# Kernel optimization log

Hardware: AMD Instinct MI355X
Metric: run time of the kernel (lower is better)

## Reference

```python
import jax, jax.numpy as jnp
import numpy as np

RES_W, RES_H = 256, 256
MAX_SAMPLES = 384
TF_RES = 128
FOV_DEG = 30.0
NEAR, FAR = 0.1, 100.0
BG = 0.0
HIT_EPS = 1e-3


def _normalize(v, axis=-1):
    return v / jnp.linalg.norm(v, axis=axis, keepdims=True)


def trilinear_sample(vol, tex):
    # vol: [X,Y,Z], tex: [...,3] in voxel coordinates
    res = np.array(vol.shape, dtype=np.float32)
    p = jnp.clip(tex, 0.0, jnp.asarray(res - 1.0 - 1e-6, jnp.float32))
    lo = jnp.floor(p).astype(jnp.int32)
    f = p - lo.astype(p.dtype)
    hi = jnp.minimum(lo + 1, jnp.asarray(res.astype(np.int32) - 1))
    x0, y0, z0 = lo[..., 0], lo[..., 1], lo[..., 2]
    x1, y1, z1 = hi[..., 0], hi[..., 1], hi[..., 2]
    fx, fy, fz = f[..., 0], f[..., 1], f[..., 2]
    c000 = vol[x0, y0, z0]; c100 = vol[x1, y0, z0]
    c010 = vol[x0, y1, z0]; c110 = vol[x1, y1, z0]
    c001 = vol[x0, y0, z1]; c101 = vol[x1, y0, z1]
    c011 = vol[x0, y1, z1]; c111 = vol[x1, y1, z1]
    c00 = c000 * (1 - fx) + c100 * fx
    c10 = c010 * (1 - fx) + c110 * fx
    c01 = c001 * (1 - fx) + c101 * fx
    c11 = c011 * (1 - fx) + c111 * fx
    c0 = c00 * (1 - fy) + c10 * fy
    c1 = c01 * (1 - fy) + c11 * fy
    return c0 * (1 - fz) + c1 * fz


def tf_lookup(tf, x):
    # tf: [T,4], x: [...] intensity in [0,1]
    T = tf.shape[0]
    xi = jnp.clip(x, 0.0, 1.0) * (T - 1)
    lo = jnp.floor(xi).astype(jnp.int32)
    hi = jnp.minimum(lo + 1, T - 1)
    f = (xi - lo.astype(xi.dtype))[..., None]
    return tf[lo] * (1 - f) + tf[hi] * f


def render_one(vol, tf, cam, sr):
    # vol [X,Y,Z], tf [T,4], cam [3] -> [W,H,5] (rgba + depth)
    W, H = RES_W, RES_H
    fwd = _normalize(-cam)
    world_up = jnp.array([0.0, 1.0, 0.0], jnp.float32)
    right = _normalize(jnp.cross(fwd, world_up))
    up = jnp.cross(right, fwd)
    tanf = jnp.tan(jnp.float32(np.radians(FOV_DEG) / 2))
    aspect = W / H
    u = ((jnp.arange(W) + 0.5) / W * 2 - 1) * tanf * aspect  # [W]
    v = ((jnp.arange(H) + 0.5) / H * 2 - 1) * tanf           # [H]
    dirs = fwd + u[:, None, None] * right + v[None, :, None] * up  # [W,H,3]
    dirs = _normalize(dirs)
    # ray-box intersection against [-1,1]^3
    inv = 1.0 / dirs
    t_lo = (-1.0 - cam) * inv
    t_hi = (1.0 - cam) * inv
    tmin = jnp.max(jnp.minimum(t_lo, t_hi), axis=-1)
    tmax = jnp.min(jnp.maximum(t_lo, t_hi), axis=-1)
    hit = (tmax >= 0.0) & (tmin <= tmax)
    entry = jnp.maximum(tmin, NEAR)
    dist = jnp.where(hit, jnp.maximum(tmax - entry, 0.0), 0.0)
    vol_max = max(vol.shape)
    # Nyquist: step = voxel size (2/vol_max) / sampling_rate
    ns = jnp.clip(jnp.ceil(dist * 0.5 * vol_max * sr), 1.0, MAX_SAMPLES)
    step = dist / ns
    k = jnp.arange(MAX_SAMPLES, dtype=jnp.float32)
    t = entry[..., None] + (k + 0.5) * step[..., None]            # [W,H,S]
    valid = (k < ns[..., None]) & hit[..., None]
    pos = cam + t[..., None] * dirs[..., None, :]                 # [W,H,S,3]
    res_m1 = jnp.asarray(np.array(vol.shape, np.float32) - 1.0)
    tex = (pos * 0.5 + 0.5) * res_m1
    intensity = trilinear_sample(vol, tex)                        # [W,H,S]
    rgba = tf_lookup(tf, intensity)                               # [W,H,S,4]
    a = rgba[..., 3]
    a = 1.0 - (1.0 - a) ** (1.0 / sr)   # opacity correction for sampling rate
    a = jnp.where(valid, a, 0.0)
    one_m = 1.0 - a
    cp = jnp.cumprod(one_m, axis=-1)
    T_excl = jnp.concatenate([jnp.ones_like(cp[..., :1]), cp[..., :-1]], axis=-1)
    w = T_excl * a                                                # [W,H,S]
    rgb = jnp.einsum('whs,whsc->whc', w, rgba[..., :3])
    acc = jnp.sum(w, axis=-1)
    rgb_out = rgb + (1.0 - acc)[..., None] * BG
    # FirstHitDepth
    hit_s = a > HIT_EPS
    any_hit = jnp.any(hit_s, axis=-1)
    first = jnp.argmax(hit_s, axis=-1)
    t_first = jnp.take_along_axis(t, first[..., None], axis=-1)[..., 0]
    depth = jnp.where(any_hit, (t_first - NEAR) / (FAR - NEAR), 1.0)
    return jnp.concatenate([rgb_out, acc[..., None], depth[..., None]], axis=-1)


def setup_inputs() -> dict:
    key = jax.random.key(0)
    k1, k2, k3 = jax.random.split(key, 3)
    volume = jax.random.uniform(k1, (1, 256, 256, 256), dtype=jnp.float32)
    tf = jax.random.uniform(k2, (1, TF_RES, 4), dtype=jnp.float32)
    look_from = jnp.array([[0.9, 0.7, -2.2]], jnp.float32) + 0.1 * jax.random.normal(k3, (1, 3), dtype=jnp.float32)
    return {"volume": volume, "tf": tf, "look_from": look_from, "sampling_rate": 1}


def reference(volume, tf, look_from, sampling_rate):
    sr = float(sampling_rate)
    return jax.vmap(lambda v, t, c: render_one(v, t, c, sr))(volume, tf, look_from)
```

## Files before the change

kernel.cpp:

```cpp
#include <hip/hip_runtime.h>
#include <math.h>

#define RES_W 256
#define RES_H 256
#define TF_RES 128

__global__ __launch_bounds__(256, 8) void raycast_kernel(
    const float* __restrict__ vol,
    const float* __restrict__ tf,
    const float* __restrict__ cam_p,
    const int*   __restrict__ sr_p,
    float* __restrict__ out)
{
    #pragma clang fp contract(off)

    __shared__ float tfR[TF_RES], tfG[TF_RES], tfB[TF_RES], tfA[TF_RES];
    const int tid = (int)threadIdx.x;
    if (tid < TF_RES) {
        float4 e = ((const float4*)tf)[tid];
        tfR[tid] = e.x; tfG[tid] = e.y; tfB[tid] = e.z; tfA[tid] = e.w;
    }
    __syncthreads();

    const int lane = tid & 63;
    const int sub  = lane & 31;

    const int b  = (int)blockIdx.x;
    const int sb = (b & 7) * 1024 + (b >> 3);
    const int ray = sb * 8 + (tid >> 5);
    const int h = ray & 255;
    const int w = ray >> 8;

    const float cx = cam_p[0], cy = cam_p[1], cz = cam_p[2];
    const int   sr_i = sr_p[0];
    const float srf = (float)sr_i;

    float nx = -cx, ny = -cy, nz = -cz;
    float fl = __fsqrt_rn((nx*nx + ny*ny) + nz*nz);
    float fx = nx / fl, fy = ny / fl, fz = nz / fl;
    float rxu = 0.0f - fz;
    float rzu = fx;
    float rl = __fsqrt_rn((rxu*rxu + 0.0f) + rzu*rzu);
    float rx = rxu / rl, rz = rzu / rl;
    float ux = 0.0f - rz*fy;
    float uy = rz*fx - rx*fz;
    float uz = rx*fy;

    const float ang32 = (float)((30.0 * 0.017453292519943295) * 0.5);
    const float tan_half = (float)tan((double)ang32);

    float uu = ((((float)w + 0.5f) / 256.0f) * 2.0f - 1.0f) * tan_half;
    float vv = ((((float)h + 0.5f) / 256.0f) * 2.0f - 1.0f) * tan_half;

    float dx = (fx + uu*rx) + vv*ux;
    float dy = (fy + 0.0f ) + vv*uy;
    float dz = (fz + uu*rz) + vv*uz;
    float dl = __fsqrt_rn((dx*dx + dy*dy) + dz*dz);
    dx = dx / dl; dy = dy / dl; dz = dz / dl;

    float ivx = 1.0f/dx, ivy = 1.0f/dy, ivz = 1.0f/dz;
    float tlx = (-1.0f - cx)*ivx, thx = (1.0f - cx)*ivx;
    float tly = (-1.0f - cy)*ivy, thy = (1.0f - cy)*ivy;
    float tlz = (-1.0f - cz)*ivz, thz = (1.0f - cz)*ivz;
    float tmin = fmaxf(fmaxf(fminf(tlx,thx), fminf(tly,thy)), fminf(tlz,thz));
    float tmax = fminf(fminf(fmaxf(tlx,thx), fmaxf(tly,thy)), fmaxf(tlz,thz));
    bool hit = (tmax >= 0.0f) && (tmin <= tmax);

    float entry = fmaxf(tmin, 0.1f);
    float dist  = hit ? fmaxf(tmax - entry, 0.0f) : 0.0f;
    float nsf   = fminf(fmaxf(ceilf(((dist * 0.5f) * 256.0f) * srf), 1.0f), 384.0f);
    int   ns    = (int)nsf;
    float step  = dist / nsf;

    float rgb_r = 0.0f, rgb_g = 0.0f, rgb_b = 0.0f, acc = 0.0f;
    float T_prev = 1.0f;
    float depth = 1.0f;
    bool  found = false;

    for (int base = 0; ; ) {
        const int  k     = base + sub;
        const bool valid = hit && (k < ns);

        float t  = entry + ((float)k + 0.5f) * step;
        float px = (cx + t*dx);
        float py = (cy + t*dy);
        float pz = (cz + t*dz);
        px = ((px * 0.5f) + 0.5f) * 255.0f;
        py = ((py * 0.5f) + 0.5f) * 255.0f;
        pz = ((pz * 0.5f) + 0.5f) * 255.0f;
        px = fminf(fmaxf(px, 0.0f), 255.0f);
        py = fminf(fmaxf(py, 0.0f), 255.0f);
        pz = fminf(fmaxf(pz, 0.0f), 255.0f);
        int x0 = (int)floorf(px), y0 = (int)floorf(py), z0 = (int)floorf(pz);
        float ffx = px - (float)x0;
        float ffy = py - (float)y0;
        float ffz = pz - (float)z0;
        int x1 = min(x0 + 1, 255);
        int y1 = min(y0 + 1, 255);
        int z1 = min(z0 + 1, 255);
        int bx0 = x0 << 16, bx1 = x1 << 16;
        int by0 = y0 << 8,  by1 = y1 << 8;
        float c000 = vol[bx0 + by0 + z0];
        float c100 = vol[bx1 + by0 + z0];
        float c010 = vol[bx0 + by1 + z0];
        float c110 = vol[bx1 + by1 + z0];
        float c001 = vol[bx0 + by0 + z1];
        float c101 = vol[bx1 + by0 + z1];
        float c011 = vol[bx0 + by1 + z1];
        float c111 = vol[bx1 + by1 + z1];

        float omx = 1.0f - ffx, omy = 1.0f - ffy, omz = 1.0f - ffz;
        float c00 = c000*omx + c100*ffx;
        float c10 = c010*omx + c110*ffx;
        float c01 = c001*omx + c101*ffx;
        float c11 = c011*omx + c111*ffx;
        float c0  = c00*omy + c10*ffy;
        float c1  = c01*omy + c11*ffy;
        float intensity = c0*omz + c1*ffz;

        float xi = fminf(fmaxf(intensity, 0.0f), 1.0f) * 127.0f;
        int lo  = (int)floorf(xi);
        int hi2 = min(lo + 1, 127);
        float tfr = xi - (float)lo;
        float omt = 1.0f - tfr;
        float cr  = tfR[lo]*omt + tfR[hi2]*tfr;
        float cg  = tfG[lo]*omt + tfG[hi2]*tfr;
        float cbb = tfB[lo]*omt + tfB[hi2]*tfr;
        float a   = tfA[lo]*omt + tfA[hi2]*tfr;

        if (sr_i == 1) {
            a = 1.0f - (1.0f - a);
        } else {
            a = 1.0f - powf(1.0f - a, 1.0f / srf);
        }
        if (!valid) a = 0.0f;
        float one_m = 1.0f - a;

        float x = one_m;
        #pragma unroll
        for (int off = 1; off < 32; off <<= 1) {
            float y = __shfl_up(x, off);
            if (sub >= off) x *= y;
        }
        float ex = __shfl_up(x, 1);
        if (sub == 0) ex = 1.0f;

        float wgt = (T_prev * ex) * a;
        float pr = wgt * cr, pg = wgt * cg, pb = wgt * cbb, pa = wgt;
        #pragma unroll
        for (int m = 16; m >= 1; m >>= 1) {
            pr += __shfl_xor(pr, m);
            pg += __shfl_xor(pg, m);
            pb += __shfl_xor(pb, m);
            pa += __shfl_xor(pa, m);
        }
        rgb_r += pr; rgb_g += pg; rgb_b += pb; acc += pa;

        int hk = (valid && (a > 1e-3f)) ? k : 0x7FFFFFFF;
        #pragma unroll
        for (int m = 16; m >= 1; m >>= 1) hk = min(hk, __shfl_xor(hk, m));
        if (!found && hk != 0x7FFFFFFF) {
            found = true;
            float tfh = entry + ((float)hk + 0.5f) * step;
            depth = (tfh - 0.1f) / 99.9f;
        }

        float Tc = __shfl(x, (lane & 32) | 31);
        T_prev = T_prev * Tc;

        base += 32;
        bool active = hit && (base < ns) && (T_prev >= 1e-7f);
        if (__ballot(active) == 0ULL) break;
    }

    if (sub == 0) {
        int oi = (w * RES_H + h) * 5;
        out[oi + 0] = rgb_r;
        out[oi + 1] = rgb_g;
        out[oi + 2] = rgb_b;
        out[oi + 3] = acc;
        out[oi + 4] = depth;
    }
}

extern "C" void kernel_launch(void* const* d_in, const int* in_sizes, int n_in,
                              void* d_out, int out_size, void* d_ws, size_t ws_size,
                              hipStream_t stream) {
    const float* vol = (const float*)d_in[0];
    const float* tf  = (const float*)d_in[1];
    const float* cam = (const float*)d_in[2];
    const int*   sr  = (const int*)d_in[3];
    float* out = (float*)d_out;

    raycast_kernel<<<dim3(8192), dim3(256), 0, stream>>>(vol, tf, cam, sr, out);
}
```

Measured before the change: 116.5 us.

## Pair z-neighbour loads, pad TF table, defer cross-lane reductions to loop end

Fetches the two z-adjacent voxels with one 8-byte load per corner pair, halving the global load instructions per sample. The transfer-function table gets a duplicated last entry so the upper-index clamp disappears. The per-iteration shuffle reductions for colour, alpha and first-hit index become per-lane accumulators that are reduced once after the loop. This removes about 25 shuffles per iteration, but changes the floating-point summation order and relies on unaligned 8-byte loads.

```diff
diff --git a/kernel.cpp b/kernel.cpp
--- a/kernel.cpp
+++ b/kernel.cpp
@@ -4,6 +4,8 @@
 #define RES_W 256
 #define RES_H 256
 #define TF_RES 128
+
+typedef float float2u __attribute__((ext_vector_type(2), aligned(4)));
 
 __global__ __launch_bounds__(256, 8) void raycast_kernel(
     const float* __restrict__ vol,
@@ -14,11 +16,14 @@
 {
     #pragma clang fp contract(off)
 
-    __shared__ float tfR[TF_RES], tfG[TF_RES], tfB[TF_RES], tfA[TF_RES];
+    __shared__ float tfR[TF_RES + 1], tfG[TF_RES + 1], tfB[TF_RES + 1], tfA[TF_RES + 1];
     const int tid = (int)threadIdx.x;
     if (tid < TF_RES) {
         float4 e = ((const float4*)tf)[tid];
         tfR[tid] = e.x; tfG[tid] = e.y; tfB[tid] = e.z; tfA[tid] = e.w;
+        if (tid == TF_RES - 1) {
+            tfR[TF_RES] = e.x; tfG[TF_RES] = e.y; tfB[TF_RES] = e.z; tfA[TF_RES] = e.w;
+        }
     }
     __syncthreads();
 
@@ -74,8 +79,7 @@
 
     float rgb_r = 0.0f, rgb_g = 0.0f, rgb_b = 0.0f, acc = 0.0f;
     float T_prev = 1.0f;
-    float depth = 1.0f;
-    bool  found = false;
+    int   hk_min = 0x7FFFFFFF;
 
     for (int base = 0; ; ) {
         const int  k     = base + sub;
@@ -97,17 +101,18 @@
         float ffz = pz - (float)z0;
         int x1 = min(x0 + 1, 255);
         int y1 = min(y0 + 1, 255);
-        int z1 = min(z0 + 1, 255);
+        int zb = min(z0, 254);
         int bx0 = x0 << 16, bx1 = x1 << 16;
         int by0 = y0 << 8,  by1 = y1 << 8;
-        float c000 = vol[bx0 + by0 + z0];
-        float c100 = vol[bx1 + by0 + z0];
-        float c010 = vol[bx0 + by1 + z0];
-        float c110 = vol[bx1 + by1 + z0];
-        float c001 = vol[bx0 + by0 + z1];
-        float c101 = vol[bx1 + by0 + z1];
-        float c011 = vol[bx0 + by1 + z1];
-        float c111 = vol[bx1 + by1 + z1];
+        float2u p00 = *(const float2u*)(vol + (bx0 + by0 + zb));
+        float2u p10 = *(const float2u*)(vol + (bx1 + by0 + zb));
+        float2u p01 = *(const float2u*)(vol + (bx0 + by1 + zb));
+        float2u p11 = *(const float2u*)(vol + (bx1 + by1 + zb));
+        bool ztop = (z0 == 255);
+        float c000 = ztop ? p00.y : p00.x;   float c001 = p00.y;
+        float c100 = ztop ? p10.y : p10.x;   float c101 = p10.y;
+        float c010 = ztop ? p01.y : p01.x;   float c011 = p01.y;
+        float c110 = ztop ? p11.y : p11.x;   float c111 = p11.y;
 
         float omx = 1.0f - ffx, omy = 1.0f - ffy, omz = 1.0f - ffz;
         float c00 = c000*omx + c100*ffx;
@@ -120,13 +125,16 @@
 
         float xi = fminf(fmaxf(intensity, 0.0f), 1.0f) * 127.0f;
         int lo  = (int)floorf(xi);
-        int hi2 = min(lo + 1, 127);
         float tfr = xi - (float)lo;
         float omt = 1.0f - tfr;
-        float cr  = tfR[lo]*omt + tfR[hi2]*tfr;
-        float cg  = tfG[lo]*omt + tfG[hi2]*tfr;
-        float cbb = tfB[lo]*omt + tfB[hi2]*tfr;
-        float a   = tfA[lo]*omt + tfA[hi2]*tfr;
+        float r0 = tfR[lo], r1 = tfR[lo + 1];
+        float g0 = tfG[lo], g1 = tfG[lo + 1];
+        float b0 = tfB[lo], b1 = tfB[lo + 1];
+        float a0 = tfA[lo], a1 = tfA[lo + 1];
+        float cr  = r0*omt + r1*tfr;
+        float cg  = g0*omt + g1*tfr;
+        float cbb = b0*omt + b1*tfr;
+        float a   = a0*omt + a1*tfr;
 
         if (sr_i == 1) {
             a = 1.0f - (1.0f - a);
@@ -146,24 +154,11 @@
         if (sub == 0) ex = 1.0f;
 
         float wgt = (T_prev * ex) * a;
-        float pr = wgt * cr, pg = wgt * cg, pb = wgt * cbb, pa = wgt;
-        #pragma unroll
-        for (int m = 16; m >= 1; m >>= 1) {
-            pr += __shfl_xor(pr, m);
-            pg += __shfl_xor(pg, m);
-            pb += __shfl_xor(pb, m);
-            pa += __shfl_xor(pa, m);
-        }
-        rgb_r += pr; rgb_g += pg; rgb_b += pb; acc += pa;
-
-        int hk = (valid && (a > 1e-3f)) ? k : 0x7FFFFFFF;
-        #pragma unroll
-        for (int m = 16; m >= 1; m >>= 1) hk = min(hk, __shfl_xor(hk, m));
-        if (!found && hk != 0x7FFFFFFF) {
-            found = true;
-            float tfh = entry + ((float)hk + 0.5f) * step;
-            depth = (tfh - 0.1f) / 99.9f;
-        }
+        rgb_r += wgt * cr;
+        rgb_g += wgt * cg;
+        rgb_b += wgt * cbb;
+        acc   += wgt;
+        if (valid && (a > 1e-3f)) hk_min = min(hk_min, k);
 
         float Tc = __shfl(x, (lane & 32) | 31);
         T_prev = T_prev * Tc;
@@ -173,7 +168,21 @@
         if (__ballot(active) == 0ULL) break;
     }
 
+    #pragma unroll
+    for (int m = 16; m >= 1; m >>= 1) {
+        rgb_r += __shfl_xor(rgb_r, m);
+        rgb_g += __shfl_xor(rgb_g, m);
+        rgb_b += __shfl_xor(rgb_b, m);
+        acc   += __shfl_xor(acc,   m);
+        hk_min = min(hk_min, __shfl_xor(hk_min, m));
+    }
+
     if (sub == 0) {
+        float depth = 1.0f;
+        if (hk_min != 0x7FFFFFFF) {
+            float tfh = entry + ((float)hk_min + 0.5f) * step;
+            depth = (tfh - 0.1f) / 99.9f;
+        }
         int oi = (w * RES_H + h) * 5;
         out[oi + 0] = rgb_r;
         out[oi + 1] = rgb_g;
```

Result: faster. 113.7 us (-2.5%).
